# Kernel optimization log

Hardware: AMD Instinct MI355X
Metric: run time of the kernel (lower is better)

The kernel has to match this reference:

```python
import jax, jax.numpy as jnp
import numpy as np

K = 2          # kernel_size
NQ = 4         # n_qubits = K*K
NL = 2         # n_layers


def setup_inputs() -> dict:
    key = jax.random.key(0)
    ks = jax.random.split(key, 6)
    x = jax.random.uniform(ks[0], (64, 1, 128, 128), jnp.float32, 0.0, np.pi)
    conv_w = jax.random.normal(ks[1], (1, 1, K, K), jnp.float32) * 0.5
    conv_b = jax.random.normal(ks[2], (1,), jnp.float32) * 0.1
    ry_angles = jax.random.normal(ks[3], (NL, NQ), jnp.float32)  # fixed RY params
    head_w = jax.random.normal(ks[4], (1, 2), jnp.float32) * 0.5
    head_b = jax.random.normal(ks[5], (1,), jnp.float32) * 0.1
    return {"x": x, "conv_w": conv_w, "conv_b": conv_b,
            "ry_angles": ry_angles, "head_w": head_w, "head_b": head_b}


def _rx(state, theta, wire):
    # state: (N, 2,2,2,2) complex; theta: (N,) batched angle
    ax = wire + 1
    st = jnp.moveaxis(state, ax, 1)
    s0, s1 = st[:, 0], st[:, 1]                      # (N, 2,2,2)
    c = jnp.cos(theta * 0.5).reshape((-1, 1, 1, 1))
    s = jnp.sin(theta * 0.5).reshape((-1, 1, 1, 1))
    n0 = c * s0 - 1j * s * s1
    n1 = -1j * s * s0 + c * s1
    return jnp.moveaxis(jnp.stack([n0, n1], axis=1), 1, ax)


def _ry(state, phi, wire):
    # phi: scalar shared angle
    ax = wire + 1
    st = jnp.moveaxis(state, ax, 1)
    s0, s1 = st[:, 0], st[:, 1]
    c = jnp.cos(phi * 0.5)
    s = jnp.sin(phi * 0.5)
    n0 = c * s0 - s * s1
    n1 = s * s0 + c * s1
    return jnp.moveaxis(jnp.stack([n0, n1], axis=1), 1, ax)


def _cnot(state, ctrl, tgt):
    ca, ta = ctrl + 1, tgt + 1
    st = jnp.moveaxis(state, (ca, ta), (1, 2))       # (N, 2, 2, rest)
    new = jnp.stack([st[:, 0], st[:, 1, ::-1]], axis=1)  # flip target where ctrl=1
    return jnp.moveaxis(new, (1, 2), (ca, ta))


def _quantum_expval_z0(patch_flat, ry_angles):
    # patch_flat: (N, 4) -> expval PauliZ(wire 0), shape (N,)
    N = patch_flat.shape[0]
    state = jnp.zeros((N, 2, 2, 2, 2), jnp.complex64).at[:, 0, 0, 0, 0].set(1.0)
    for w in range(NQ):
        state = _rx(state, patch_flat[:, w], w)
    for l in range(NL):
        for w in range(NQ):
            state = _ry(state, ry_angles[l, w], w)
        for w in range(0, NQ - 1, 2):
            state = _cnot(state, w, w + 1)
    p = jnp.real(state) ** 2 + jnp.imag(state) ** 2   # (N,2,2,2,2)
    return p[:, 0].sum(axis=(1, 2, 3)) - p[:, 1].sum(axis=(1, 2, 3))


def reference(x, conv_w, conv_b, ry_angles, head_w, head_b):
    B, _, H, W = x.shape
    # all KxK sliding patches, feature order (c, kh, kw) row-major == patch.view(-1)
    patches = jax.lax.conv_general_dilated_patches(x, (K, K), (1, 1), 'VALID')  # (B,4,Ph,Pw)
    Ph, Pw = patches.shape[2], patches.shape[3]
    pf = patches.transpose(0, 2, 3, 1).reshape(-1, K * K)   # (N, 4)
    conv_out = pf @ conv_w.reshape(K * K) + conv_b[0]       # (N,)
    q_out = _quantum_expval_z0(pf, ry_angles)               # (N,)
    per_patch = head_w[0, 0] * conv_out + head_w[0, 1] * q_out + head_b[0]
    out = per_patch.reshape(B, Ph * Pw).mean(axis=1)        # mean over windows
    return out[:, None]
```

## Files before the change

### kernel.cpp

```cpp
#include <hip/hip_runtime.h>
#include <math.h>


#define XW 128
#define NP (127 * 127)
#define NB 64
#define RPB 4
#define NBLK 32
#define BLK 256

__device__ __forceinline__ void circuit_coeffs(const float* __restrict__ ry,
                                               float k[5]) {
    float U[4][4] = {{1,0,0,0},{0,1,0,0},{0,0,1,0},{0,0,0,1}};
    for (int l = 0; l < 2; ++l) {
        float s0, c0, s1, c1;
        __sincosf(0.5f * ry[l*4+0], &s0, &c0);
        __sincosf(0.5f * ry[l*4+1], &s1, &c1);
        for (int q1 = 0; q1 < 2; ++q1)
            for (int c = 0; c < 4; ++c) {
                float a = U[q1][c], d = U[2+q1][c];
                U[q1][c]   = c0*a - s0*d;
                U[2+q1][c] = s0*a + c0*d;
            }
        for (int m = 0; m < 2; ++m)
            for (int c = 0; c < 4; ++c) {
                float a = U[2*m][c], d = U[2*m+1][c];
                U[2*m][c]   = c1*a - s1*d;
                U[2*m+1][c] = s1*a + c1*d;
            }
        for (int c = 0; c < 4; ++c) { float t = U[2][c]; U[2][c] = U[3][c]; U[3][c] = t; }
    }
    float pA=0, pB=0, pC=0, pD=0, pAD=0, pBC=0;
    for (int r = 0; r < 4; ++r) {
        float g = (r < 2) ? 1.f : -1.f;
        pA  += g * U[r][0] * U[r][0];
        pB  += g * U[r][1] * U[r][1];
        pC  += g * U[r][2] * U[r][2];
        pD  += g * U[r][3] * U[r][3];
        pAD += g * U[r][0] * U[r][3];
        pBC += g * U[r][1] * U[r][2];
    }
    k[0] = 0.25f * (pA + pB + pC + pD);
    k[1] = 0.25f * (pA + pB - pC - pD);
    k[2] = 0.25f * (pA - pB + pC - pD);
    k[3] = 0.25f * (pA - pB - pC + pD);
    k[4] = 0.50f * (pBC - pAD);
}

__global__ __launch_bounds__(BLK) void row_kernel(
    const float* __restrict__ x,
    const float* __restrict__ conv_w,
    const float* __restrict__ head_w,
    const float* __restrict__ ry,
    float* __restrict__ part)
{
    __shared__ float red[BLK / 64];

    const int tid  = threadIdx.x;
    const int lane = tid & 63;
    const int wave = tid >> 6;
    const int img  = blockIdx.y;
    const int row  = blockIdx.x * RPB + wave;

    float k[5];
    circuit_coeffs(ry, k);
    const float hw0 = head_w[0], hw1 = head_w[1];
    const float k1 = hw1 * k[1], k2 = hw1 * k[2];
    const float k3 = hw1 * k[3], k4 = hw1 * k[4];
    const float w0 = hw0 * conv_w[0], w1 = hw0 * conv_w[1];
    const float w2 = hw0 * conv_w[2], w3 = hw0 * conv_w[3];

    const float P = (row < 127 ? w0 : 0.f) + (row > 0 ? w2 : 0.f);
    const float Q = (row < 127 ? w1 : 0.f) + (row > 0 ? w3 : 0.f);

    const float2* __restrict__ xr =
        (const float2*)(x + ((size_t)img * 128 + row) * XW);
    const float2 e = xr[lane];

    float acc = e.x * (P + (lane > 0 ? Q : 0.f))
              + e.y * (Q + (lane < 63 ? P : 0.f));

    if (row < 127) {
        float s0, c0, s1, c1;
        __sincosf(e.x, &s0, &c0);
        __sincosf(e.y, &s1, &c1);
        float cn = __shfl_down(c0, 1, 64);
        float sn = __shfl_down(s0, 1, 64);
        acc += k1 * c0 + k2 * c1 + k3 * c0 * c1 + k4 * s0 * s1;
        if (lane < 63)
            acc += k1 * c1 + k2 * cn + k3 * c1 * cn + k4 * s1 * sn;
    }

    for (int off = 32; off > 0; off >>= 1)
        acc += __shfl_down(acc, off, 64);
    if (lane == 0) red[wave] = acc;
    __syncthreads();
    if (tid == 0) {
        float t = red[0] + red[1] + red[2] + red[3];
        part[img * NBLK + blockIdx.x] = t;
    }
}

__global__ __launch_bounds__(64) void final_kernel(
    const float* __restrict__ part,
    const float* __restrict__ conv_b,
    const float* __restrict__ ry,
    const float* __restrict__ head_w,
    const float* __restrict__ head_b,
    float* __restrict__ out)
{
    const int b = threadIdx.x;
    float k[5];
    circuit_coeffs(ry, k);
    float sum = 0.f;
    for (int s = 0; s < NBLK; ++s) sum += part[b * NBLK + s];
    const float cconst = head_w[0] * conv_b[0] + head_w[1] * k[0] + head_b[0];
    out[b] = sum * (1.0f / NP) + cconst;
}

extern "C" void kernel_launch(void* const* d_in, const int* in_sizes, int n_in,
                              void* d_out, int out_size, void* d_ws, size_t ws_size,
                              hipStream_t stream) {
    const float* x      = (const float*)d_in[0];
    const float* conv_w = (const float*)d_in[1];
    const float* conv_b = (const float*)d_in[2];
    const float* ry     = (const float*)d_in[3];
    const float* head_w = (const float*)d_in[4];
    const float* head_b = (const float*)d_in[5];
    float* out  = (float*)d_out;
    float* part = (float*)d_ws;

    dim3 grid(NBLK, NB);
    row_kernel<<<grid, BLK, 0, stream>>>(x, conv_w, head_w, ry, part);
    final_kernel<<<1, 64, 0, stream>>>(part, conv_b, ry, head_w, head_b, out);
}
```

Baseline: 68.74 us.

## Process two rows per wave with float4 loads and compute circuit coeffs once per block

Each wave now covers two image rows, with each half-wave of 32 lanes loading a float4 per lane. This halves the block count per image and doubles the work per thread. The circuit coefficients are now computed by one thread and shared through LDS instead of being recomputed by every thread, which removes redundant transcendental math. The cost is an extra block-wide barrier, and the neighbour shuffle now crosses the half-wave boundary, where it is masked by the col0 check.

```diff
diff --git a/kernel.cpp b/kernel.cpp
--- a/kernel.cpp
+++ b/kernel.cpp
@@ -5,8 +5,7 @@
 #define XW 128
 #define NP (127 * 127)
 #define NB 64
-#define RPB 4
-#define NBLK 32
+#define NBLK 16
 #define BLK 256
 
 __device__ __forceinline__ void circuit_coeffs(const float* __restrict__ ry,
@@ -54,51 +53,64 @@
     const float* __restrict__ ry,
     float* __restrict__ part)
 {
+    __shared__ float sk[4];
     __shared__ float red[BLK / 64];
 
     const int tid  = threadIdx.x;
     const int lane = tid & 63;
     const int wave = tid >> 6;
+    const int half = lane >> 5;
+    const int col0 = (lane & 31) << 2;
     const int img  = blockIdx.y;
-    const int row  = blockIdx.x * RPB + wave;
+    const int row  = (blockIdx.x << 3) + (wave << 1) + half;
 
-    float k[5];
-    circuit_coeffs(ry, k);
-    const float hw0 = head_w[0], hw1 = head_w[1];
-    const float k1 = hw1 * k[1], k2 = hw1 * k[2];
-    const float k3 = hw1 * k[3], k4 = hw1 * k[4];
+    if (tid == 0) {
+        float k[5];
+        circuit_coeffs(ry, k);
+        const float hw1 = head_w[1];
+        sk[0] = hw1 * k[1]; sk[1] = hw1 * k[2];
+        sk[2] = hw1 * k[3]; sk[3] = hw1 * k[4];
+    }
+    __syncthreads();
+
+    const float hw0 = head_w[0];
     const float w0 = hw0 * conv_w[0], w1 = hw0 * conv_w[1];
     const float w2 = hw0 * conv_w[2], w3 = hw0 * conv_w[3];
+    const float k1 = sk[0], k2 = sk[1], k3 = sk[2], k4 = sk[3];
 
     const float P = (row < 127 ? w0 : 0.f) + (row > 0 ? w2 : 0.f);
     const float Q = (row < 127 ? w1 : 0.f) + (row > 0 ? w3 : 0.f);
+    const float PQ = P + Q;
 
-    const float2* __restrict__ xr =
-        (const float2*)(x + ((size_t)img * 128 + row) * XW);
-    const float2 e = xr[lane];
+    const float4 e = ((const float4*)(x + ((size_t)img * 128 + row) * XW))
+                         [lane & 31];
 
-    float acc = e.x * (P + (lane > 0 ? Q : 0.f))
-              + e.y * (Q + (lane < 63 ? P : 0.f));
+    float acc = e.x * (col0 == 0 ? P : PQ)
+              + e.y * PQ
+              + e.z * PQ
+              + e.w * (col0 == 124 ? Q : PQ);
 
     if (row < 127) {
-        float s0, c0, s1, c1;
+        float s0,c0,s1,c1,s2,c2,s3,c3;
         __sincosf(e.x, &s0, &c0);
         __sincosf(e.y, &s1, &c1);
-        float cn = __shfl_down(c0, 1, 64);
-        float sn = __shfl_down(s0, 1, 64);
+        __sincosf(e.z, &s2, &c2);
+        __sincosf(e.w, &s3, &c3);
+        const float cn = __shfl_down(c0, 1, 64);
+        const float sn = __shfl_down(s0, 1, 64);
         acc += k1 * c0 + k2 * c1 + k3 * c0 * c1 + k4 * s0 * s1;
-        if (lane < 63)
-            acc += k1 * c1 + k2 * cn + k3 * c1 * cn + k4 * s1 * sn;
+        acc += k1 * c1 + k2 * c2 + k3 * c1 * c2 + k4 * s1 * s2;
+        acc += k1 * c2 + k2 * c3 + k3 * c2 * c3 + k4 * s2 * s3;
+        if (col0 < 124)
+            acc += k1 * c3 + k2 * cn + k3 * c3 * cn + k4 * s3 * sn;
     }
 
     for (int off = 32; off > 0; off >>= 1)
         acc += __shfl_down(acc, off, 64);
     if (lane == 0) red[wave] = acc;
     __syncthreads();
-    if (tid == 0) {
-        float t = red[0] + red[1] + red[2] + red[3];
-        part[img * NBLK + blockIdx.x] = t;
-    }
+    if (tid == 0)
+        part[img * NBLK + blockIdx.x] = red[0] + red[1] + red[2] + red[3];
 }
 
 __global__ __launch_bounds__(64) void final_kernel(
```

After: 65.43 us. 4.8% less time.
